# Kernel optimization log

Measured on AMD Instinct MI355X. Metric: run time of the kernel, lower is better.

The kernel has to match this reference:

```python
import jax, jax.numpy as jnp
import numpy as np

BOUND = 1.2


def _ste_sign(v, bound):
    # forward: sign(v); backward: d clamp(v,-bound,bound)/dv (straight-through estimator)
    clipped = jnp.clip(v, -bound, bound)
    return jax.lax.stop_gradient(jnp.sign(v) - clipped) + clipped


def setup_inputs() -> dict:
    key = jax.random.key(0)
    kx, kw = jax.random.split(key)
    x = jax.random.normal(kx, (32, 128, 112, 112), dtype=jnp.float32)
    # xavier_normal_ with gain=2.0: std = gain * sqrt(2/(fan_in+fan_out)), fan = C*k*k
    fan = 128 * 3 * 3
    std = 2.0 * np.sqrt(2.0 / (fan + fan))
    weights = jax.random.normal(kw, (128, 128, 3, 3), dtype=jnp.float32) * std
    return {"x": x, "weights": weights}


def reference(x, weights):
    # Binarize activations and weights with STE (training-mode math of BConv)
    xb = _ste_sign(x, BOUND)
    wb = _ste_sign(weights, BOUND)
    # conv2d, NCHW input, OIHW weights, stride 1, padding 1, dilation 1
    out = jax.lax.conv_general_dilated(
        xb, wb,
        window_strides=(1, 1),
        padding=((1, 1), (1, 1)),
        lhs_dilation=(1, 1),
        rhs_dilation=(1, 1),
        dimension_numbers=("NCHW", "OIHW", "NCHW"),
        feature_group_count=1,
    )
    return out
```

## Files before the change

### kernel.cpp

```cpp
#include <hip/hip_runtime.h>
#include <cstdint>
#include <cstddef>

#define NIMG 32
#define C    128
#define OC   128
#define HW   112
#define HWSZ (HW * HW)
#define NTAP 9
#define PHW  114
#define XROW (PHW * C)
#define AWQ_BYTES ((size_t)4 * 9 * 4 * 64 * 16)

typedef int v4i  __attribute__((ext_vector_type(4)));
typedef int v16i __attribute__((ext_vector_type(16)));

__global__ void pack_w_frag(const float* __restrict__ w, uint32_t* __restrict__ awq) {
    int tid = blockIdx.x * blockDim.x + threadIdx.x;
    int d = tid & 3, l = (tid >> 2) & 63, f = tid >> 8;
    int ks = f & 3, tf = f >> 2;
    int tap = tf % 9, wv = tf / 9;
    int o = wv * 32 + (l & 31);
    int cb = ks * 32 + ((l >> 5) & 1) * 16 + d * 4;
    uint32_t acc = 0;
    #pragma unroll
    for (int jj = 0; jj < 4; ++jj) {
        uint32_t bits = __float_as_uint(w[(size_t)(o * C + cb + jj) * NTAP + tap]);
        acc |= (((bits >> 31) * 0xFEu) ^ 1u) << (8 * jj);
    }
    awq[tid] = acc;
}

__global__ __launch_bounds__(256, 2) void bconv_fused(const float* __restrict__ x,
                                                      const uint8_t* __restrict__ awq,
                                                      float* __restrict__ out) {
    __shared__ __align__(16) uint8_t sxq[4 * XROW];
    int bid = blockIdx.x;
    int swz = (bid & 7) * 224 + (bid >> 3);
    int n = swz / 56, hp = swz % 56;
    int h0 = hp * 2;

    #pragma unroll
    for (int rep = 0; rep < 2; ++rep) {
        int task = threadIdx.x + rep * 256;
        if (task < 448) {
            int r = task / 112, rem = task % 112;
            int w = rem & 3, pxg = rem >> 2;
            int hr = h0 - 1 + r;
            int col0 = 1 + pxg * 4;
            int sbase = r * XROW;
            if (hr >= 0 && hr < HW) {
                const float* xp = x + ((size_t)(n * C + w * 32)) * HWSZ
                                    + (size_t)hr * HW + pxg * 4;
                uint32_t dw[4][8];
                #pragma unroll
                for (int j = 0; j < 4; ++j)
                    #pragma unroll
                    for (int d = 0; d < 8; ++d) dw[j][d] = 0u;
                #pragma unroll
                for (int c = 0; c < 32; ++c) {
                    float4 v = *reinterpret_cast<const float4*>(xp + (size_t)c * HWSZ);
                    uint32_t bm = 0xFFu << (8 * (c & 3));
                    int d = c >> 2;
                    dw[0][d] |= ((uint32_t)((int)__float_as_uint(v.x) >> 31)) & bm;
                    dw[1][d] |= ((uint32_t)((int)__float_as_uint(v.y) >> 31)) & bm;
                    dw[2][d] |= ((uint32_t)((int)__float_as_uint(v.z) >> 31)) & bm;
                    dw[3][d] |= ((uint32_t)((int)__float_as_uint(v.w) >> 31)) & bm;
                }
                #pragma unroll
                for (int j = 0; j < 4; ++j) {
                    int col = col0 + j;
                    int c7 = col & 7;
                    int line = sbase + col * 128;
                    uint32_t d0 = (dw[j][0] & 0xFEFEFEFEu) ^ 0x01010101u;
                    uint32_t d1 = (dw[j][1] & 0xFEFEFEFEu) ^ 0x01010101u;
                    uint32_t d2 = (dw[j][2] & 0xFEFEFEFEu) ^ 0x01010101u;
                    uint32_t d3 = (dw[j][3] & 0xFEFEFEFEu) ^ 0x01010101u;
                    *(uint4*)&sxq[line + (((w)     ^ c7) << 4)] = make_uint4(d0, d1, d2, d3);
                    uint32_t d4 = (dw[j][4] & 0xFEFEFEFEu) ^ 0x01010101u;
                    uint32_t d5 = (dw[j][5] & 0xFEFEFEFEu) ^ 0x01010101u;
                    uint32_t d6 = (dw[j][6] & 0xFEFEFEFEu) ^ 0x01010101u;
                    uint32_t d7 = (dw[j][7] & 0xFEFEFEFEu) ^ 0x01010101u;
                    *(uint4*)&sxq[line + (((w + 4) ^ c7) << 4)] = make_uint4(d4, d5, d6, d7);
                }
            } else {
                #pragma unroll
                for (int j = 0; j < 4; ++j) {
                    int col = col0 + j;
                    int c7 = col & 7;
                    int line = sbase + col * 128;
                    *(uint4*)&sxq[line + (((w)     ^ c7) << 4)] = make_uint4(0u, 0u, 0u, 0u);
                    *(uint4*)&sxq[line + (((w + 4) ^ c7) << 4)] = make_uint4(0u, 0u, 0u, 0u);
                }
            }
        } else if (task < 456) {
            int j = task - 448;
            int r = j >> 1, side = j & 1;
            int col = side ? 113 : 0;
            #pragma unroll
            for (int k = 0; k < 8; ++k)
                *(uint4*)&sxq[r * XROW + col * 128 + k * 16] = make_uint4(0u, 0u, 0u, 0u);
        }
    }

    int wv = threadIdx.x >> 6, l = threadIdx.x & 63;
    int l31 = l & 31, hh = l >> 5;
    v4i A[9][4];
    #pragma unroll
    for (int tap = 0; tap < 9; ++tap)
        #pragma unroll
        for (int ks = 0; ks < 4; ++ks) {
            int f = (wv * 9 + tap) * 4 + ks;
            A[tap][ks] = *(const v4i*)(awq + (size_t)f * 1024 + (size_t)l * 16);
        }
    __syncthreads();

    float* outb = out + ((size_t)n * OC + wv * 32) * HWSZ + (size_t)h0 * HW;

    for (int nt = 0; nt < 7; ++nt) {
        int p = nt * 32 + l31;
        int rl = (p >= HW) ? 1 : 0;
        int w = p - rl * HW;

        int ad[3][4];
        #pragma unroll
        for (int kw = 0; kw < 3; ++kw) {
            int col = w + kw;
            int c7x = (col & 7) << 4;
            int b0 = rl * XROW + col * 128;
            #pragma unroll
            for (int ks = 0; ks < 4; ++ks)
                ad[kw][ks] = b0 + ((((ks + (hh << 2)) << 4)) ^ c7x);
        }

        v16i acc0 = {0,0,0,0,0,0,0,0,0,0,0,0,0,0,0,0};
        v16i acc1 = {0,0,0,0,0,0,0,0,0,0,0,0,0,0,0,0};
        #pragma unroll
        for (int kh = 0; kh < 3; ++kh)
            #pragma unroll
            for (int kw = 0; kw < 3; ++kw)
                #pragma unroll
                for (int ks = 0; ks < 4; ++ks) {
                    v4i b = *(const v4i*)&sxq[kh * XROW + ad[kw][ks]];
                    if (ks & 1)
                        acc1 = __builtin_amdgcn_mfma_i32_32x32x32_i8(
                                   A[kh * 3 + kw][ks], b, acc1, 0, 0, 0);
                    else
                        acc0 = __builtin_amdgcn_mfma_i32_32x32x32_i8(
                                   A[kh * 3 + kw][ks], b, acc0, 0, 0, 0);
                }
        v16i acc = acc0 + acc1;

        #pragma unroll
        for (int r = 0; r < 16; ++r) {
            int oof = (r & 3) + 8 * (r >> 2) + 4 * hh;
            outb[(size_t)oof * HWSZ + rl * HW + w] = (float)acc[r];
        }
    }
}

extern "C" void kernel_launch(void* const* d_in, const int* in_sizes, int n_in,
                              void* d_out, int out_size, void* d_ws, size_t ws_size,
                              hipStream_t stream) {
    const float* x   = (const float*)d_in[0];
    const float* wts = (const float*)d_in[1];
    float* out = (float*)d_out;
    uint32_t* awq = (uint32_t*)d_ws;

    hipLaunchKernelGGL(pack_w_frag, dim3(144), dim3(256), 0, stream, wts, awq);
    hipLaunchKernelGGL(bconv_fused, dim3(NIMG * 56), dim3(256), 0, stream,
                       x, (const uint8_t*)awq, out);
}
```

Measured before the change: 134.7 us.

## Switch to 16x16x64 int8 MFMA with one output row per 512-thread block

Replaces the 32x32x32 int8 MFMA with the 16x16x64 variant. Weight fragments are repacked for 16 output channels per wave, and each block now has 8 waves covering all 128 channels for a single output row. The shared tile shrinks from 4 input rows to 3, so the two-row halo overlap is dropped, but each input row is now loaded three times instead of twice. This trades more redundant global input traffic and a different occupancy profile for simpler accumulators and fewer registers per wave.

```diff
diff --git a/kernel.cpp b/kernel.cpp
--- a/kernel.cpp
+++ b/kernel.cpp
@@ -10,18 +10,17 @@
 #define NTAP 9
 #define PHW  114
 #define XROW (PHW * C)
-#define AWQ_BYTES ((size_t)4 * 9 * 4 * 64 * 16)
+#define AWQ_BYTES ((size_t)8 * 9 * 2 * 64 * 16)
 
 typedef int v4i  __attribute__((ext_vector_type(4)));
-typedef int v16i __attribute__((ext_vector_type(16)));
 
 __global__ void pack_w_frag(const float* __restrict__ w, uint32_t* __restrict__ awq) {
     int tid = blockIdx.x * blockDim.x + threadIdx.x;
     int d = tid & 3, l = (tid >> 2) & 63, f = tid >> 8;
-    int ks = f & 3, tf = f >> 2;
-    int tap = tf % 9, wv = tf / 9;
-    int o = wv * 32 + (l & 31);
-    int cb = ks * 32 + ((l >> 5) & 1) * 16 + d * 4;
+    int ks = f & 1, tf = f >> 1;
+    int tap = tf % 9, o16 = tf / 9;
+    int o = o16 * 16 + (l & 15);
+    int cb = ks * 64 + ((l >> 4) & 3) * 16 + d * 4;
     uint32_t acc = 0;
     #pragma unroll
     for (int jj = 0; jj < 4; ++jj) {
@@ -31,130 +30,117 @@
     awq[tid] = acc;
 }
 
-__global__ __launch_bounds__(256, 2) void bconv_fused(const float* __restrict__ x,
-                                                      const uint8_t* __restrict__ awq,
-                                                      float* __restrict__ out) {
-    __shared__ __align__(16) uint8_t sxq[4 * XROW];
+__global__ __launch_bounds__(512) void bconv_fused(const float* __restrict__ x,
+                                                   const uint8_t* __restrict__ awq,
+                                                   float* __restrict__ out) {
+    __shared__ __align__(16) uint8_t sxq[3 * XROW];
     int bid = blockIdx.x;
-    int swz = (bid & 7) * 224 + (bid >> 3);
-    int n = swz / 56, hp = swz % 56;
-    int h0 = hp * 2;
+    int swz = (bid & 7) * 448 + (bid >> 3);
+    int n = swz / HW, h = swz % HW;
 
-    #pragma unroll
-    for (int rep = 0; rep < 2; ++rep) {
-        int task = threadIdx.x + rep * 256;
-        if (task < 448) {
-            int r = task / 112, rem = task % 112;
-            int w = rem & 3, pxg = rem >> 2;
-            int hr = h0 - 1 + r;
-            int col0 = 1 + pxg * 4;
-            int sbase = r * XROW;
-            if (hr >= 0 && hr < HW) {
-                const float* xp = x + ((size_t)(n * C + w * 32)) * HWSZ
-                                    + (size_t)hr * HW + pxg * 4;
-                uint32_t dw[4][8];
+    int tid = threadIdx.x;
+    int wv = tid >> 6, l = tid & 63;
+
+    if (tid < 336) {
+        int r = tid / 112, rem = tid % 112;
+        int w = rem & 3, pxg = rem >> 2;
+        int hr = h - 1 + r;
+        int col0 = 1 + pxg * 4;
+        int sbase = r * XROW;
+        if (hr >= 0 && hr < HW) {
+            const float* xp = x + ((size_t)(n * C + w * 32)) * HWSZ
+                                + (size_t)hr * HW + pxg * 4;
+            uint32_t dw[4][8];
+            #pragma unroll
+            for (int j = 0; j < 4; ++j)
                 #pragma unroll
-                for (int j = 0; j < 4; ++j)
-                    #pragma unroll
-                    for (int d = 0; d < 8; ++d) dw[j][d] = 0u;
-                #pragma unroll
-                for (int c = 0; c < 32; ++c) {
-                    float4 v = *reinterpret_cast<const float4*>(xp + (size_t)c * HWSZ);
-                    uint32_t bm = 0xFFu << (8 * (c & 3));
-                    int d = c >> 2;
-                    dw[0][d] |= ((uint32_t)((int)__float_as_uint(v.x) >> 31)) & bm;
-                    dw[1][d] |= ((uint32_t)((int)__float_as_uint(v.y) >> 31)) & bm;
-                    dw[2][d] |= ((uint32_t)((int)__float_as_uint(v.z) >> 31)) & bm;
-                    dw[3][d] |= ((uint32_t)((int)__float_as_uint(v.w) >> 31)) & bm;
-                }
-                #pragma unroll
-                for (int j = 0; j < 4; ++j) {
-                    int col = col0 + j;
-                    int c7 = col & 7;
-                    int line = sbase + col * 128;
-                    uint32_t d0 = (dw[j][0] & 0xFEFEFEFEu) ^ 0x01010101u;
-                    uint32_t d1 = (dw[j][1] & 0xFEFEFEFEu) ^ 0x01010101u;
-                    uint32_t d2 = (dw[j][2] & 0xFEFEFEFEu) ^ 0x01010101u;
-                    uint32_t d3 = (dw[j][3] & 0xFEFEFEFEu) ^ 0x01010101u;
-                    *(uint4*)&sxq[line + (((w)     ^ c7) << 4)] = make_uint4(d0, d1, d2, d3);
-                    uint32_t d4 = (dw[j][4] & 0xFEFEFEFEu) ^ 0x01010101u;
-                    uint32_t d5 = (dw[j][5] & 0xFEFEFEFEu) ^ 0x01010101u;
-                    uint32_t d6 = (dw[j][6] & 0xFEFEFEFEu) ^ 0x01010101u;
-                    uint32_t d7 = (dw[j][7] & 0xFEFEFEFEu) ^ 0x01010101u;
-                    *(uint4*)&sxq[line + (((w + 4) ^ c7) << 4)] = make_uint4(d4, d5, d6, d7);
-                }
-            } else {
-                #pragma unroll
-                for (int j = 0; j < 4; ++j) {
-                    int col = col0 + j;
-                    int c7 = col & 7;
-                    int line = sbase + col * 128;
-                    *(uint4*)&sxq[line + (((w)     ^ c7) << 4)] = make_uint4(0u, 0u, 0u, 0u);
-                    *(uint4*)&sxq[line + (((w + 4) ^ c7) << 4)] = make_uint4(0u, 0u, 0u, 0u);
-                }
+                for (int d = 0; d < 8; ++d) dw[j][d] = 0u;
+            #pragma unroll
+            for (int c = 0; c < 32; ++c) {
+                float4 v = *reinterpret_cast<const float4*>(xp + (size_t)c * HWSZ);
+                uint32_t bm = 0xFFu << (8 * (c & 3));
+                int d = c >> 2;
+                dw[0][d] |= ((uint32_t)((int)__float_as_uint(v.x) >> 31)) & bm;
+                dw[1][d] |= ((uint32_t)((int)__float_as_uint(v.y) >> 31)) & bm;
+                dw[2][d] |= ((uint32_t)((int)__float_as_uint(v.z) >> 31)) & bm;
+                dw[3][d] |= ((uint32_t)((int)__float_as_uint(v.w) >> 31)) & bm;
             }
-        } else if (task < 456) {
-            int j = task - 448;
-            int r = j >> 1, side = j & 1;
-            int col = side ? 113 : 0;
             #pragma unroll
-            for (int k = 0; k < 8; ++k)
-                *(uint4*)&sxq[r * XROW + col * 128 + k * 16] = make_uint4(0u, 0u, 0u, 0u);
+            for (int j = 0; j < 4; ++j) {
+                int col = col0 + j;
+                int c7 = col & 7;
+                int line = sbase + col * 128;
+                uint32_t d0 = (dw[j][0] & 0xFEFEFEFEu) ^ 0x01010101u;
+                uint32_t d1 = (dw[j][1] & 0xFEFEFEFEu) ^ 0x01010101u;
+                uint32_t d2 = (dw[j][2] & 0xFEFEFEFEu) ^ 0x01010101u;
+                uint32_t d3 = (dw[j][3] & 0xFEFEFEFEu) ^ 0x01010101u;
+                *(uint4*)&sxq[line + (((w)     ^ c7) << 4)] = make_uint4(d0, d1, d2, d3);
+                uint32_t d4 = (dw[j][4] & 0xFEFEFEFEu) ^ 0x01010101u;
+                uint32_t d5 = (dw[j][5] & 0xFEFEFEFEu) ^ 0x01010101u;
+                uint32_t d6 = (dw[j][6] & 0xFEFEFEFEu) ^ 0x01010101u;
+                uint32_t d7 = (dw[j][7] & 0xFEFEFEFEu) ^ 0x01010101u;
+                *(uint4*)&sxq[line + (((w + 4) ^ c7) << 4)] = make_uint4(d4, d5, d6, d7);
+            }
+        } else {
+            #pragma unroll
+            for (int j = 0; j < 4; ++j) {
+                int col = col0 + j;
+                int c7 = col & 7;
+                int line = sbase + col * 128;
+                *(uint4*)&sxq[line + (((w)     ^ c7) << 4)] = make_uint4(0u, 0u, 0u, 0u);
+                *(uint4*)&sxq[line + (((w + 4) ^ c7) << 4)] = make_uint4(0u, 0u, 0u, 0u);
+            }
         }
+    } else if (tid < 384) {
+        int j = tid - 336;
+        int r = j >> 4, side = (j >> 3) & 1, k = j & 7;
+        int col = side ? 113 : 0;
+        *(uint4*)&sxq[r * XROW + col * 128 + k * 16] = make_uint4(0u, 0u, 0u, 0u);
     }
 
-    int wv = threadIdx.x >> 6, l = threadIdx.x & 63;
-    int l31 = l & 31, hh = l >> 5;
-    v4i A[9][4];
+    v4i A[9][2];
     #pragma unroll
     for (int tap = 0; tap < 9; ++tap)
         #pragma unroll
-        for (int ks = 0; ks < 4; ++ks) {
-            int f = (wv * 9 + tap) * 4 + ks;
+        for (int ks = 0; ks < 2; ++ks) {
+            int f = (wv * 9 + tap) * 2 + ks;
             A[tap][ks] = *(const v4i*)(awq + (size_t)f * 1024 + (size_t)l * 16);
         }
     __syncthreads();
 
-    float* outb = out + ((size_t)n * OC + wv * 32) * HWSZ + (size_t)h0 * HW;
+    int l15 = l & 15, g = l >> 4;
+    float* outb = out + ((size_t)n * OC + wv * 16) * HWSZ + (size_t)h * HW;
 
     for (int nt = 0; nt < 7; ++nt) {
-        int p = nt * 32 + l31;
-        int rl = (p >= HW) ? 1 : 0;
-        int w = p - rl * HW;
+        int px = nt * 16 + l15;
 
-        int ad[3][4];
+        int sbase0 = (g >> 1) + 4 * (g & 1);
+        int ad[3][2];
         #pragma unroll
         for (int kw = 0; kw < 3; ++kw) {
-            int col = w + kw;
-            int c7x = (col & 7) << 4;
-            int b0 = rl * XROW + col * 128;
-            #pragma unroll
-            for (int ks = 0; ks < 4; ++ks)
-                ad[kw][ks] = b0 + ((((ks + (hh << 2)) << 4)) ^ c7x);
+            int col = px + kw;
+            int c7 = col & 7;
+            int line = col * 128;
+            ad[kw][0] = line + (((sbase0)     ^ c7) << 4);
+            ad[kw][1] = line + (((sbase0 + 2) ^ c7) << 4);
         }
 
-        v16i acc0 = {0,0,0,0,0,0,0,0,0,0,0,0,0,0,0,0};
-        v16i acc1 = {0,0,0,0,0,0,0,0,0,0,0,0,0,0,0,0};
+        v4i acc = {0, 0, 0, 0};
         #pragma unroll
         for (int kh = 0; kh < 3; ++kh)
             #pragma unroll
             for (int kw = 0; kw < 3; ++kw)
                 #pragma unroll
-                for (int ks = 0; ks < 4; ++ks) {
+                for (int ks = 0; ks < 2; ++ks) {
                     v4i b = *(const v4i*)&sxq[kh * XROW + ad[kw][ks]];
-                    if (ks & 1)
-                        acc1 = __builtin_amdgcn_mfma_i32_32x32x32_i8(
-                                   A[kh * 3 + kw][ks], b, acc1, 0, 0, 0);
-                    else
-                        acc0 = __builtin_amdgcn_mfma_i32_32x32x32_i8(
-                                   A[kh * 3 + kw][ks], b, acc0, 0, 0, 0);
+                    acc = __builtin_amdgcn_mfma_i32_16x16x64_i8(
+                              A[kh * 3 + kw][ks], b, acc, 0, 0, 0);
                 }
-        v16i acc = acc0 + acc1;
 
         #pragma unroll
-        for (int r = 0; r < 16; ++r) {
-            int oof = (r & 3) + 8 * (r >> 2) + 4 * hh;
-            outb[(size_t)oof * HWSZ + rl * HW + w] = (float)acc[r];
+        for (int r = 0; r < 4; ++r) {
+            int oof = g * 4 + r;
+            outb[(size_t)oof * HWSZ + px] = (float)acc[r];
         }
     }
 }
@@ -168,6 +154,6 @@
     uint32_t* awq = (uint32_t*)d_ws;
 
     hipLaunchKernelGGL(pack_w_frag, dim3(144), dim3(256), 0, stream, wts, awq);
-    hipLaunchKernelGGL(bconv_fused, dim3(NIMG * 56), dim3(256), 0, stream,
+    hipLaunchKernelGGL(bconv_fused, dim3(NIMG * HW), dim3(512), 0, stream,
                        x, (const uint8_t*)awq, out);
 }
```

After: 191.4 us. 1.42x slower.
